# Performance work log

Hardware: AMD Instinct MI355X
Metric: run time of the kernel (lower is better)

## Reference

```python
import jax, jax.numpy as jnp
import numpy as np
from jax import lax

NPOINT = 1024
RADIUS = 0.4
NSAMPLE = 32
BN_EPS = 1e-5


def _square_distance(src, dst):
    # src [B,S,3], dst [B,N,3] -> [B,S,N]
    d = -2.0 * jnp.einsum('bsc,bnc->bsn', src, dst)
    d = d + jnp.sum(src ** 2, -1)[:, :, None]
    d = d + jnp.sum(dst ** 2, -1)[:, None, :]
    return d


def _farthest_point_sample(xyz, npoint):
    # xyz [B,N,3] -> int32 indices [B,npoint]
    B, N, _ = xyz.shape
    # deterministic start at index 0 (torch uses randint; math is otherwise identical)
    init_far = jnp.zeros((B,), dtype=jnp.int32)
    init_dist = jnp.full((B, N), 1e10, dtype=xyz.dtype)

    def step(carry, _):
        distance, farthest = carry
        centroid = jnp.take_along_axis(xyz, farthest[:, None, None], axis=1)  # [B,1,3]
        dist = jnp.sum((xyz - centroid) ** 2, -1)  # [B,N]
        distance = jnp.minimum(distance, dist)
        new_far = jnp.argmax(distance, axis=-1).astype(jnp.int32)
        return (distance, new_far), farthest

    (_, _), cents = lax.scan(step, (init_dist, init_far), None, length=npoint)
    return cents.T  # [B, npoint]


def _query_ball_point(radius, nsample, xyz, new_xyz):
    # xyz [B,N,3], new_xyz [B,S,3] -> idx [B,S,nsample]
    B, N, _ = xyz.shape
    sqr = _square_distance(new_xyz, xyz)  # [B,S,N]
    ar = jnp.arange(N, dtype=jnp.int32)
    gi = jnp.where(sqr > radius * radius, N, ar[None, None, :])
    gi = jnp.sort(gi, axis=-1)[:, :, :nsample]
    first = gi[:, :, :1]
    return jnp.where(gi == N, first, gi)


def setup_inputs() -> dict:
    key = jax.random.key(0)
    ks = jax.random.split(key, 8)
    B, N = 16, 4096
    inp = {
        'xyz': jax.random.normal(ks[0], (B, 3, N), jnp.float32),
        'points': jax.random.normal(ks[1], (B, 6, N), jnp.float32),
    }
    dims = [(64, 9), (64, 64), (128, 64)]
    for i, (o, c) in enumerate(dims):
        inp[f'w{i}'] = jax.random.normal(ks[2 + i], (o, c), jnp.float32) * 0.05
        inp[f'b{i}'] = jnp.zeros((o,), jnp.float32)
        inp[f'g{i}'] = jnp.ones((o,), jnp.float32)
        inp[f'beta{i}'] = jnp.zeros((o,), jnp.float32)
    return inp


def reference(xyz, points, w0, b0, g0, beta0, w1, b1, g1, beta1, w2, b2, g2, beta2):
    # xyz [B,3,N], points [B,6,N]
    xyz_t = jnp.transpose(xyz, (0, 2, 1))      # [B,N,3]
    pts_t = jnp.transpose(points, (0, 2, 1))   # [B,N,6]
    B, N, _ = xyz_t.shape
    S, ns = NPOINT, NSAMPLE

    fps_idx = _farthest_point_sample(xyz_t, S)                 # [B,S]
    new_xyz = jnp.take_along_axis(xyz_t, fps_idx[:, :, None], axis=1)  # [B,S,3]
    idx = _query_ball_point(RADIUS, ns, xyz_t, new_xyz)        # [B,S,ns]
    flat = idx.reshape(B, S * ns, 1)
    g_xyz = jnp.take_along_axis(xyz_t, flat, axis=1).reshape(B, S, ns, 3)
    g_xyz = g_xyz - new_xyz[:, :, None, :]                     # grouped_xyz_norm
    g_pts = jnp.take_along_axis(pts_t, flat, axis=1).reshape(B, S, ns, -1)
    feat = jnp.concatenate([g_xyz, g_pts], axis=-1)            # [B,S,ns,9]

    # shared MLP: 1x1 conv + BatchNorm (training-mode batch stats) + ReLU
    for w, b, g, be in ((w0, b0, g0, beta0), (w1, b1, g1, beta1), (w2, b2, g2, beta2)):
        h = jnp.einsum('bsnc,oc->bsno', feat, w) + b
        mu = jnp.mean(h, axis=(0, 1, 2))
        var = jnp.var(h, axis=(0, 1, 2))
        feat = jax.nn.relu((h - mu) * lax.rsqrt(var + BN_EPS) * g + be)

    new_points = jnp.max(feat, axis=2)                         # max over nsample -> [B,S,Cout]
    return (jnp.transpose(new_xyz, (0, 2, 1)), jnp.transpose(new_points, (0, 2, 1)))
```

## Files before the change

### kernel.cpp

```cpp
#include <hip/hip_runtime.h>
#include <hip/hip_bf16.h>
#include <stdint.h>

#define NB 16
#define NP 4096
#define NSP 1024
#define KNN 32
#define PTOT (NB*NSP*KNN)
#define NTILES (PTOT/16)

typedef __attribute__((ext_vector_type(8))) short short8;
typedef __attribute__((ext_vector_type(4))) float f32x4;
typedef __attribute__((ext_vector_type(2))) float f32x2;

__device__ __forceinline__ float fadd_(float a,float b){return __fadd_rn(a,b);}
__device__ __forceinline__ float fmul_(float a,float b){return __fmul_rn(a,b);}
__device__ __forceinline__ float fsub_(float a,float b){return __fsub_rn(a,b);}

__device__ __forceinline__ float bf2f(unsigned short u){
    unsigned int x = ((unsigned int)u) << 16; float f; __builtin_memcpy(&f,&x,4); return f;
}
__device__ __forceinline__ unsigned short f2bf(float f){
    unsigned int x; __builtin_memcpy(&x,&f,4);
    x = x + 0x7fffu + ((x>>16)&1u);
    return (unsigned short)(x>>16);
}

template<int CTRL>
__device__ __forceinline__ float dpp_fmax_step(float v){
    int d = __builtin_amdgcn_update_dpp(0, __float_as_int(v), CTRL, 0xF, 0xF, true);
    return fmaxf(v, __int_as_float(d));
}

__device__ __forceinline__ void ab_from_stats(const double* __restrict__ st, const float* __restrict__ g,
    const float* __restrict__ beta, int o, float* A_out, float* B_out)
{
    double s=0.0, q=0.0;
#pragma unroll
    for (int slot=0;slot<8;slot++){
        s += st[(size_t)(slot*2+0)*128+o];
        q += st[(size_t)(slot*2+1)*128+o];
    }
    const double cnt = (double)PTOT;
    float mean = (float)(s/cnt);
    float var  = (float)(q/cnt - (s/cnt)*(s/cnt));
    float inv  = rsqrtf(var + 1e-5f);
    float A = g[o]*inv;
    *A_out = A; *B_out = beta[o] - mean*A;
}

__global__ __launch_bounds__(256,1) void fps_kernel(const float* __restrict__ xyz,
    float* __restrict__ new_xyz, float* __restrict__ out0)
{
    const int b = blockIdx.x, tid = threadIdx.x;
    const int lane = tid & 63, wv = tid >> 6;
    const float* xb = xyz + (size_t)b*3*NP;
    __shared__ float4 sp[NP];
    __shared__ unsigned long long slots[2][4];
    __shared__ int lds_far[NSP];
    f32x2 px[8], py[8], pz[8], pd2[8];
    const int base = tid*16;
#pragma unroll
    for (int j=0;j<16;j+=4){
        float4 vx = *(const float4*)(xb + base + j);
        float4 vy = *(const float4*)(xb + NP + base + j);
        float4 vz = *(const float4*)(xb + 2*NP + base + j);
        px[j/2]   = (f32x2){vx.x,vx.y}; px[j/2+1] = (f32x2){vx.z,vx.w};
        py[j/2]   = (f32x2){vy.x,vy.y}; py[j/2+1] = (f32x2){vy.z,vy.w};
        pz[j/2]   = (f32x2){vz.x,vz.y}; pz[j/2+1] = (f32x2){vz.z,vz.w};
        sp[base+j+0] = make_float4(vx.x,vy.x,vz.x,0.f);
        sp[base+j+1] = make_float4(vx.y,vy.y,vz.y,0.f);
        sp[base+j+2] = make_float4(vx.z,vy.z,vz.z,0.f);
        sp[base+j+3] = make_float4(vx.w,vy.w,vz.w,0.f);
        pd2[j/2]   = (f32x2){1e10f,1e10f};
        pd2[j/2+1] = (f32x2){1e10f,1e10f};
    }
    __syncthreads();
    int far = 0;
    float cx, cy, cz;
    { float4 c0 = sp[0]; cx=c0.x; cy=c0.y; cz=c0.z; }
    for (int s=0;s<NSP;s++){
        if (tid == (s & 255)) lds_far[s] = far;
        f32x2 bm2 = (f32x2){-1.f,-1.f};
        {
#pragma clang fp contract(off)
            const f32x2 cx2 = (f32x2){cx,cx}, cy2 = (f32x2){cy,cy}, cz2 = (f32x2){cz,cz};
#pragma unroll
            for (int k=0;k<8;k++){
                f32x2 dx = px[k]-cx2, dy = py[k]-cy2, dz = pz[k]-cz2;
                f32x2 d  = (dx*dx + dy*dy) + dz*dz;
                pd2[k] = __builtin_elementwise_min(pd2[k], d);
                bm2    = __builtin_elementwise_max(bm2, pd2[k]);
            }
        }
        float bd = fmaxf(bm2.x, bm2.y);
        float m = bd;
        m = dpp_fmax_step<0x111>(m);
        m = dpp_fmax_step<0x112>(m);
        m = dpp_fmax_step<0x114>(m);
        m = dpp_fmax_step<0x118>(m);
        m = dpp_fmax_step<0x142>(m);
        m = dpp_fmax_step<0x143>(m);
        const float wm = __int_as_float(__builtin_amdgcn_readlane(__float_as_int(m), 63));
        int il = 0;
#pragma unroll
        for (int k=7;k>=0;k--){
            if (pd2[k].y == wm) il = 2*k+1;
            if (pd2[k].x == wm) il = 2*k;
        }
        unsigned long long wmask = __ballot(bd == wm);
        int L = __ffsll(wmask) - 1;
        int widx = __builtin_amdgcn_readlane(base + il, L);
        unsigned long long key = ((unsigned long long)__float_as_uint(wm) << 32)
                               | (unsigned int)(NP-1-widx);
        if (lane==0) slots[s&1][wv] = key;
        __syncthreads();
        {
            const unsigned long long* sl = slots[s&1];
            unsigned long long a0 = sl[0], a1 = sl[1], a2 = sl[2], a3 = sl[3];
            unsigned long long m0 = a0>a1?a0:a1, m1 = a2>a3?a2:a3;
            unsigned long long mx = m0>m1?m0:m1;
            far = NP-1-(int)(mx & 0xFFFFFFFFu);
        }
        float4 c = sp[far]; cx=c.x; cy=c.y; cz=c.z;
    }
    __syncthreads();
    for (int i=tid;i<NSP;i+=256){
        int id = lds_far[i];
        float4 c = sp[id];
        float* nz = new_xyz + ((size_t)b*NSP + i)*3;
        nz[0]=c.x; nz[1]=c.y; nz[2]=c.z;
        out0[(size_t)b*3*NSP + i]         = c.x;
        out0[(size_t)b*3*NSP + NSP + i]   = c.y;
        out0[(size_t)b*3*NSP + 2*NSP + i] = c.z;
    }
}

__global__ __launch_bounds__(256,1) void ball_gather_kernel(const float* __restrict__ xyz,
    const float* __restrict__ pts, const float* __restrict__ new_xyz,
    unsigned short* __restrict__ feat)
{
    const int lane = threadIdx.x & 63, wv = threadIdx.x >> 6;
    const int center = blockIdx.x*4 + wv;
    const int b = center >> 10;
    const float* xb = xyz + (size_t)b*3*NP;
    const float* pb = pts + (size_t)b*6*NP;
    const float* nz = new_xyz + (size_t)center*3;
    const float cx=nz[0], cy=nz[1], cz=nz[2];
    const float src2 = fadd_(fadd_(fmul_(cx,cx),fmul_(cy,cy)),fmul_(cz,cz));
    const float R2 = (float)(0.4*0.4);
    __shared__ int slots[4][32];
    int total = 0;
    for (int c0=0;c0<NP;c0+=64){
        const int i = c0 + lane;
        float x=xb[i], y=xb[NP+i], z=xb[2*NP+i];
        float dot  = fadd_(fadd_(fmul_(cx,x),fmul_(cy,y)),fmul_(cz,z));
        float dst2 = fadd_(fadd_(fmul_(x,x),fmul_(y,y)),fmul_(z,z));
        float d = fadd_(fadd_(fmul_(-2.0f,dot), src2), dst2);
        bool pred = !(d > R2);
        unsigned long long m = __ballot(pred);
        int pos = total + (int)__popcll(m & ((1ull<<lane)-1ull));
        if (pred && pos < 32) slots[wv][pos] = i;
        total += (int)__popcll(m);
        if (total >= 32) break;
    }
    const int nvalid = total < 32 ? total : 32;
    const int n = lane & 31;
    const int idx = slots[wv][ (n < nvalid) ? n : 0 ];
    unsigned short* fr = feat + (size_t)center*KNN*32 + (size_t)n*32;
    if (lane < 32){
        float gx = fsub_(xb[idx], cx), gy = fsub_(xb[NP+idx], cy), gz = fsub_(xb[2*NP+idx], cz);
        float p0=pb[idx], p1=pb[NP+idx], p2=pb[2*NP+idx], p3=pb[3*NP+idx], p4=pb[4*NP+idx];
        short8 v;
        v[0]=(short)f2bf(gx); v[1]=(short)f2bf(gy); v[2]=(short)f2bf(gz);
        v[3]=(short)f2bf(p0); v[4]=(short)f2bf(p1); v[5]=(short)f2bf(p2);
        v[6]=(short)f2bf(p3); v[7]=(short)f2bf(p4);
        *(short8*)fr = v;
    } else {
        float p5 = pb[5*NP+idx];
        short8 v = (short8){0,0,0,0,0,0,0,0};
        v[0]=(short)f2bf(p5);
        *(short8*)(fr+8)  = v;
        short8 z8 = (short8){0,0,0,0,0,0,0,0};
        *(short8*)(fr+16) = z8;
        *(short8*)(fr+24) = z8;
    }
}

template<int KT,int OT,bool NORM_IN,bool STORE_H>
__global__ __launch_bounds__(256,1) void conv_kernel(const unsigned short* __restrict__ in,
    const unsigned short* __restrict__ wp, const float* __restrict__ bias,
    const double* __restrict__ stats_in, const float* __restrict__ gin,
    const float* __restrict__ bein,
    unsigned short* __restrict__ h_out, double* __restrict__ stats)
{
    constexpr int K = KT*32, O = OT*16;
    const int lane = threadIdx.x & 63, wv = threadIdx.x >> 6;
    const int col = lane & 15, quad = lane >> 4;
    __shared__ float sA[128], sB[128];
    if constexpr (NORM_IN){
        if ((int)threadIdx.x < K){
            float A, B;
            ab_from_stats(stats_in, gin, bein, threadIdx.x, &A, &B);
            sA[threadIdx.x] = A; sB[threadIdx.x] = B;
        }
        __syncthreads();
    }
    short8 bf[OT][KT];
#pragma unroll
    for (int t=0;t<OT;t++)
#pragma unroll
        for (int kt=0;kt<KT;kt++)
            bf[t][kt] = *(const short8*)(wp + (size_t)(t*16+col)*K + kt*32 + quad*8);
    float brow[OT];
#pragma unroll
    for (int t=0;t<OT;t++) brow[t] = bias[t*16+col];
    float nA[KT*8], nB[KT*8];
    if constexpr (NORM_IN){
#pragma unroll
        for (int kt=0;kt<KT;kt++)
#pragma unroll
            for (int j=0;j<8;j++){
                int c = kt*32+quad*8+j;
                nA[kt*8+j]=sA[c]; nB[kt*8+j]=sB[c];
            }
    }
    float ssum[OT], ssq[OT];
#pragma unroll
    for (int t=0;t<OT;t++){ ssum[t]=0.f; ssq[t]=0.f; }
    const int gw = blockIdx.x*4 + wv, nw = gridDim.x*4;
    for (int tile=gw; tile<NTILES; tile+=nw){
        const int row0 = tile*16;
        short8 af[KT];
#pragma unroll
        for (int kt=0;kt<KT;kt++){
            af[kt] = *(const short8*)(in + (size_t)(row0+col)*K + kt*32 + quad*8);
            if constexpr (NORM_IN){
#pragma unroll
                for (int j=0;j<8;j++){
                    float x = bf2f((unsigned short)af[kt][j]);
                    x = fmaxf(x*nA[kt*8+j]+nB[kt*8+j], 0.f);
                    af[kt][j] = (short)f2bf(x);
                }
            }
        }
        f32x4 acc[OT];
#pragma unroll
        for (int t=0;t<OT;t++) acc[t] = (f32x4){0.f,0.f,0.f,0.f};
#pragma unroll
        for (int kt=0;kt<KT;kt++)
#pragma unroll
            for (int t=0;t<OT;t++)
                acc[t] = __builtin_amdgcn_mfma_f32_16x16x32_bf16(af[kt], bf[t][kt], acc[t], 0,0,0);
#pragma unroll
        for (int t=0;t<OT;t++){
#pragma unroll
            for (int r=0;r<4;r++){
                float h = acc[t][r] + brow[t];
                if constexpr (STORE_H)
                    h_out[(size_t)(row0 + quad*4 + r)*O + t*16 + col] = f2bf(h);
                ssum[t] += h; ssq[t] = fmaf(h,h,ssq[t]);
            }
        }
    }
    __shared__ float bsum[128], bssq[128];
    for (int i=threadIdx.x;i<128;i+=256){ bsum[i]=0.f; bssq[i]=0.f; }
    __syncthreads();
#pragma unroll
    for (int t=0;t<OT;t++){
        float v = ssum[t]; v += __shfl_xor(v,16,64); v += __shfl_xor(v,32,64);
        float q = ssq[t];  q += __shfl_xor(q,16,64); q += __shfl_xor(q,32,64);
        if (quad==0){ atomicAdd(&bsum[t*16+col], v); atomicAdd(&bssq[t*16+col], q); }
    }
    __syncthreads();
    if ((int)threadIdx.x < O){
        const int slot = blockIdx.x & 7;
        atomicAdd(&stats[(size_t)(slot*2+0)*128 + threadIdx.x], (double)bsum[threadIdx.x]);
        atomicAdd(&stats[(size_t)(slot*2+1)*128 + threadIdx.x], (double)bssq[threadIdx.x]);
    }
}

__global__ __launch_bounds__(256,1) void conv_final_kernel(const unsigned short* __restrict__ in,
    const unsigned short* __restrict__ wp, const float* __restrict__ bias,
    const double* __restrict__ stats1, const float* __restrict__ g1v,
    const float* __restrict__ be1v,
    const double* __restrict__ stats2, const float* __restrict__ g2v,
    const float* __restrict__ be2v,
    float* __restrict__ out1)
{
    constexpr int KT=2, OT=8, K=64;
    const int lane = threadIdx.x & 63, wv = threadIdx.x >> 6;
    const int col = lane & 15, quad = lane >> 4;
    __shared__ float sInA[64], sInB[64], sOutA[128], sOutB[128];
    {
        const int t0 = threadIdx.x;
        if (t0 < 128){
            float A, B;
            ab_from_stats(stats2, g2v, be2v, t0, &A, &B);
            sOutA[t0] = A; sOutB[t0] = B;
        } else if (t0 < 192){
            float A, B;
            ab_from_stats(stats1, g1v, be1v, t0-128, &A, &B);
            sInA[t0-128] = A; sInB[t0-128] = B;
        }
        __syncthreads();
    }
    short8 bf[OT][KT];
#pragma unroll
    for (int t=0;t<OT;t++)
#pragma unroll
        for (int kt=0;kt<KT;kt++)
            bf[t][kt] = *(const short8*)(wp + (size_t)(t*16+col)*K + kt*32 + quad*8);
    float brow[OT], oA[OT], oB[OT];
#pragma unroll
    for (int t=0;t<OT;t++){
        brow[t] = bias[t*16+col];
        oA[t] = sOutA[t*16+col];
        oB[t] = sOutB[t*16+col];
    }
    float nA[16], nB[16];
#pragma unroll
    for (int kt=0;kt<2;kt++)
#pragma unroll
        for (int j=0;j<8;j++){
            int c = kt*32+quad*8+j;
            nA[kt*8+j]=sInA[c]; nB[kt*8+j]=sInB[c];
        }
    const int gw = blockIdx.x*4 + wv, nw = gridDim.x*4;
    for (int grp=gw; grp<NB*NSP; grp+=nw){
        float vmax[OT];
#pragma unroll
        for (int t=0;t<OT;t++) vmax[t]=0.f;
#pragma unroll
        for (int mt=0; mt<2; mt++){
            const int row0 = grp*32 + mt*16;
            short8 af[KT];
#pragma unroll
            for (int kt=0;kt<2;kt++){
                af[kt] = *(const short8*)(in + (size_t)(row0+col)*K + kt*32 + quad*8);
#pragma unroll
                for (int j=0;j<8;j++){
                    float x = bf2f((unsigned short)af[kt][j]);
                    x = fmaxf(x*nA[kt*8+j]+nB[kt*8+j], 0.f);
                    af[kt][j] = (short)f2bf(x);
                }
            }
            f32x4 acc[OT];
#pragma unroll
            for (int t=0;t<OT;t++) acc[t] = (f32x4){0.f,0.f,0.f,0.f};
#pragma unroll
            for (int kt=0;kt<2;kt++)
#pragma unroll
                for (int t=0;t<OT;t++)
                    acc[t] = __builtin_amdgcn_mfma_f32_16x16x32_bf16(af[kt], bf[t][kt], acc[t], 0,0,0);
#pragma unroll
            for (int t=0;t<OT;t++){
#pragma unroll
                for (int r=0;r<4;r++){
                    float h = acc[t][r] + brow[t];
                    float x = fmaxf(h*oA[t]+oB[t], 0.f);
                    vmax[t] = fmaxf(vmax[t], x);
                }
            }
        }
#pragma unroll
        for (int t=0;t<OT;t++){
            float v = vmax[t];
            v = fmaxf(v, __shfl_xor(v,16,64));
            v = fmaxf(v, __shfl_xor(v,32,64));
            if (quad==0){
                int o = t*16+col, bb = grp>>10, ss = grp&1023;
                out1[((size_t)bb*128+o)*NSP + ss] = v;
            }
        }
    }
}

__global__ void prep_kernel(const float* __restrict__ w0, const float* __restrict__ w1,
    const float* __restrict__ w2, unsigned short* __restrict__ wp0,
    unsigned short* __restrict__ wp1, unsigned short* __restrict__ wp2)
{
    int t = blockIdx.x*256 + threadIdx.x;
    if (t < 64*32){ int o=t>>5, c=t&31; wp0[t] = (c<9) ? f2bf(w0[o*9+c]) : (unsigned short)0; }
    if (t < 64*64)  wp1[t] = f2bf(w1[t]);
    if (t < 128*64) wp2[t] = f2bf(w2[t]);
}

extern "C" void kernel_launch(void* const* d_in, const int* in_sizes, int n_in,
                              void* d_out, int out_size, void* d_ws, size_t ws_size,
                              hipStream_t stream)
{
    (void)in_sizes; (void)n_in; (void)out_size; (void)ws_size;
    const float* xyz = (const float*)d_in[0];
    const float* pts = (const float*)d_in[1];
    const float* w0  = (const float*)d_in[2];
    const float* b0  = (const float*)d_in[3];
    const float* g0  = (const float*)d_in[4];
    const float* be0 = (const float*)d_in[5];
    const float* w1  = (const float*)d_in[6];
    const float* b1  = (const float*)d_in[7];
    const float* g1  = (const float*)d_in[8];
    const float* be1 = (const float*)d_in[9];
    const float* w2  = (const float*)d_in[10];
    const float* b2  = (const float*)d_in[11];
    const float* g2  = (const float*)d_in[12];
    const float* be2 = (const float*)d_in[13];

    char* ws = (char*)d_ws;
    size_t off = 0;
    auto alloc = [&](size_t sz)->char*{ char* p = ws + off; off = (off + sz + 255) & ~(size_t)255; return p; };
    float*          new_xyz = (float*)         alloc((size_t)NB*NSP*3*4);
    unsigned short* wp0     = (unsigned short*)alloc(64*32*2);
    unsigned short* wp1     = (unsigned short*)alloc(64*64*2);
    unsigned short* wp2     = (unsigned short*)alloc(128*64*2);
    double*         stats   = (double*)        alloc((size_t)3*8*2*128*8);
    unsigned short* feat    = (unsigned short*)alloc((size_t)PTOT*32*2);
    unsigned short* h0      = (unsigned short*)alloc((size_t)PTOT*64*2);
    unsigned short* h1      = (unsigned short*)alloc((size_t)PTOT*64*2);

    float* out0 = (float*)d_out;
    float* out1 = out0 + (size_t)NB*3*NSP;

    hipMemsetAsync(stats, 0, (size_t)3*8*2*128*8, stream);
    prep_kernel<<<32,256,0,stream>>>(w0,w1,w2,wp0,wp1,wp2);
    fps_kernel<<<NB,256,0,stream>>>(xyz, new_xyz, out0);
    ball_gather_kernel<<<NB*NSP/4,256,0,stream>>>(xyz, pts, new_xyz, feat);
    conv_kernel<1,4,false,true><<<1024,256,0,stream>>>(feat, wp0, b0, nullptr, nullptr, nullptr, h0, stats);
    conv_kernel<2,4,true,true><<<1024,256,0,stream>>>(h0, wp1, b1, stats, g0, be0, h1, stats + 2048);
    conv_kernel<2,8,true,false><<<1024,256,0,stream>>>(h1, wp2, b2, stats + 2048, g1, be1, nullptr, stats + 4096);
    conv_final_kernel<<<2048,256,0,stream>>>(h1, wp2, b2, stats + 2048, g1, be1, stats + 4096, g2, be2, out1);
}
```

Measured before the change: 868.6 us.

## Fuse layer-0 recompute with layer-1 conv to drop h0 intermediate buffer

The first conv pass now only computes batch statistics and no longer writes h0. A new fused kernel recomputes layer 0 from feat, applies BN+ReLU in registers and LDS scratch, and feeds the result straight into the layer-1 MFMA, writing h1 and its stats. This removes the write and read of the 64-channel bf16 h0 tensor (about 67MB each way) at the cost of recomputing the small K=32 layer-0 matmul.

```diff
diff --git a/kernel.cpp b/kernel.cpp
--- a/kernel.cpp
+++ b/kernel.cpp
@@ -280,6 +280,102 @@
     }
 }
 
+__global__ __launch_bounds__(256,1) void conv01_kernel(
+    const unsigned short* __restrict__ feat,
+    const unsigned short* __restrict__ wp0, const float* __restrict__ b0v,
+    const double* __restrict__ stats0, const float* __restrict__ g0v,
+    const float* __restrict__ be0v,
+    const unsigned short* __restrict__ wp1, const float* __restrict__ b1v,
+    unsigned short* __restrict__ h1_out, double* __restrict__ stats1)
+{
+    const int lane = threadIdx.x & 63, wv = threadIdx.x >> 6;
+    const int col = lane & 15, quad = lane >> 4;
+    __shared__ float sA[64], sB[64];
+    __shared__ unsigned short scratch[4][16*72];
+    if ((int)threadIdx.x < 64){
+        float A, B;
+        ab_from_stats(stats0, g0v, be0v, threadIdx.x, &A, &B);
+        sA[threadIdx.x] = A; sB[threadIdx.x] = B;
+    }
+    __syncthreads();
+    short8 bf0[4];
+#pragma unroll
+    for (int t=0;t<4;t++)
+        bf0[t] = *(const short8*)(wp0 + (size_t)(t*16+col)*32 + quad*8);
+    short8 bf1[4][2];
+#pragma unroll
+    for (int t=0;t<4;t++)
+#pragma unroll
+        for (int kt=0;kt<2;kt++)
+            bf1[t][kt] = *(const short8*)(wp1 + (size_t)(t*16+col)*64 + kt*32 + quad*8);
+    float b0row[4], n0A[4], n0B[4], b1row[4];
+#pragma unroll
+    for (int t=0;t<4;t++){
+        b0row[t] = b0v[t*16+col];
+        n0A[t]   = sA[t*16+col];
+        n0B[t]   = sB[t*16+col];
+        b1row[t] = b1v[t*16+col];
+    }
+    float ssum[4], ssq[4];
+#pragma unroll
+    for (int t=0;t<4;t++){ ssum[t]=0.f; ssq[t]=0.f; }
+    unsigned short* sw = scratch[wv];
+    const int gw = blockIdx.x*4 + wv, nw = gridDim.x*4;
+    for (int tile=gw; tile<NTILES; tile+=nw){
+        const int row0 = tile*16;
+        short8 af0 = *(const short8*)(feat + (size_t)(row0+col)*32 + quad*8);
+        f32x4 acc0[4];
+#pragma unroll
+        for (int t=0;t<4;t++) acc0[t] = (f32x4){0.f,0.f,0.f,0.f};
+#pragma unroll
+        for (int t=0;t<4;t++)
+            acc0[t] = __builtin_amdgcn_mfma_f32_16x16x32_bf16(af0, bf0[t], acc0[t], 0,0,0);
+#pragma unroll
+        for (int t=0;t<4;t++)
+#pragma unroll
+            for (int r=0;r<4;r++){
+                float h = acc0[t][r] + b0row[t];
+                unsigned short hb = f2bf(h);
+                float x = fmaxf(bf2f(hb)*n0A[t] + n0B[t], 0.f);
+                sw[(quad*4+r)*72 + t*16 + col] = f2bf(x);
+            }
+        short8 af1[2];
+        af1[0] = *(const short8*)(&sw[(size_t)col*72 + quad*8]);
+        af1[1] = *(const short8*)(&sw[(size_t)col*72 + 32 + quad*8]);
+        f32x4 acc1[4];
+#pragma unroll
+        for (int t=0;t<4;t++) acc1[t] = (f32x4){0.f,0.f,0.f,0.f};
+#pragma unroll
+        for (int kt=0;kt<2;kt++)
+#pragma unroll
+            for (int t=0;t<4;t++)
+                acc1[t] = __builtin_amdgcn_mfma_f32_16x16x32_bf16(af1[kt], bf1[t][kt], acc1[t], 0,0,0);
+#pragma unroll
+        for (int t=0;t<4;t++)
+#pragma unroll
+            for (int r=0;r<4;r++){
+                float h = acc1[t][r] + b1row[t];
+                h1_out[(size_t)(row0 + quad*4 + r)*64 + t*16 + col] = f2bf(h);
+                ssum[t] += h; ssq[t] = fmaf(h,h,ssq[t]);
+            }
+    }
+    __shared__ float bsum[64], bssq[64];
+    for (int i=threadIdx.x;i<64;i+=256){ bsum[i]=0.f; bssq[i]=0.f; }
+    __syncthreads();
+#pragma unroll
+    for (int t=0;t<4;t++){
+        float v = ssum[t]; v += __shfl_xor(v,16,64); v += __shfl_xor(v,32,64);
+        float q = ssq[t];  q += __shfl_xor(q,16,64); q += __shfl_xor(q,32,64);
+        if (quad==0){ atomicAdd(&bsum[t*16+col], v); atomicAdd(&bssq[t*16+col], q); }
+    }
+    __syncthreads();
+    if ((int)threadIdx.x < 64){
+        const int slot = blockIdx.x & 7;
+        atomicAdd(&stats1[(size_t)(slot*2+0)*128 + threadIdx.x], (double)bsum[threadIdx.x]);
+        atomicAdd(&stats1[(size_t)(slot*2+1)*128 + threadIdx.x], (double)bssq[threadIdx.x]);
+    }
+}
+
 __global__ __launch_bounds__(256,1) void conv_final_kernel(const unsigned short* __restrict__ in,
     const unsigned short* __restrict__ wp, const float* __restrict__ bias,
     const double* __restrict__ stats1, const float* __restrict__ g1v,
@@ -415,7 +511,6 @@
     unsigned short* wp2     = (unsigned short*)alloc(128*64*2);
     double*         stats   = (double*)        alloc((size_t)3*8*2*128*8);
     unsigned short* feat    = (unsigned short*)alloc((size_t)PTOT*32*2);
-    unsigned short* h0      = (unsigned short*)alloc((size_t)PTOT*64*2);
     unsigned short* h1      = (unsigned short*)alloc((size_t)PTOT*64*2);
 
     float* out0 = (float*)d_out;
@@ -425,8 +520,8 @@
     prep_kernel<<<32,256,0,stream>>>(w0,w1,w2,wp0,wp1,wp2);
     fps_kernel<<<NB,256,0,stream>>>(xyz, new_xyz, out0);
     ball_gather_kernel<<<NB*NSP/4,256,0,stream>>>(xyz, pts, new_xyz, feat);
-    conv_kernel<1,4,false,true><<<1024,256,0,stream>>>(feat, wp0, b0, nullptr, nullptr, nullptr, h0, stats);
-    conv_kernel<2,4,true,true><<<1024,256,0,stream>>>(h0, wp1, b1, stats, g0, be0, h1, stats + 2048);
+    conv_kernel<1,4,false,false><<<1024,256,0,stream>>>(feat, wp0, b0, nullptr, nullptr, nullptr, nullptr, stats);
+    conv01_kernel<<<1024,256,0,stream>>>(feat, wp0, b0, stats, g0, be0, wp1, b1, h1, stats + 2048);
     conv_kernel<2,8,true,false><<<1024,256,0,stream>>>(h1, wp2, b2, stats + 2048, g1, be1, nullptr, stats + 4096);
     conv_final_kernel<<<2048,256,0,stream>>>(h1, wp2, b2, stats + 2048, g1, be1, stats + 4096, g2, be2, out1);
 }
```

Measured after the change: 860.8 us, median of 2. Within noise of the previous version (-0.9%).
